# Kernel tuning notes

Measured on AMD Instinct MI355X. Metric: run time of the kernel, lower is better.

Reference implementation:

```python
import jax, jax.numpy as jnp
import numpy as np

B, T, D = 2, 2048, 2048
H, KV, HD = 16, 8, 128
N_REP = H // KV
EPS = 1e-6
ROPE_THETA = 5e6
K_MASK = float(jnp.finfo(jnp.bfloat16).min)


def setup_inputs() -> dict:
    key = jax.random.key(0)
    ks = jax.random.split(key, 8)
    x = jax.random.normal(ks[0], (B, T, D), dtype=jnp.float32)
    wq = jax.random.normal(ks[1], (D, H * HD), dtype=jnp.float32) * 0.02
    wk = jax.random.normal(ks[2], (D, KV * HD), dtype=jnp.float32) * 0.02
    wv = jax.random.normal(ks[3], (D, KV * HD), dtype=jnp.float32) * 0.02
    wo = jax.random.normal(ks[4], (H * HD, D), dtype=jnp.float32) * 0.02
    qn_w = jnp.ones((HD,), dtype=jnp.float32)
    kn_w = jnp.ones((HD,), dtype=jnp.float32)
    # real rotary angles: [T, HD//2] -> broadcast to [B, T, HD//2]
    pos = jnp.arange(T, dtype=jnp.float32)
    inv_freq = 1.0 / (ROPE_THETA ** (jnp.arange(0, HD, 2, dtype=jnp.float32) / HD))
    ang = pos[:, None] * inv_freq[None, :]
    sin = jnp.broadcast_to(jnp.sin(ang)[None], (B, T, HD // 2))
    cos = jnp.broadcast_to(jnp.cos(ang)[None], (B, T, HD // 2))
    # causal mask [B, 1, T, T]
    causal = jnp.tril(jnp.ones((T, T), dtype=jnp.bool_))
    mask = jnp.broadcast_to(causal[None, None], (B, 1, T, T))
    k_cache = jnp.zeros((B, T, KV, HD), dtype=jnp.float32)
    v_cache = jnp.zeros((B, T, KV, HD), dtype=jnp.float32)
    return {"x": x, "wq": wq, "wk": wk, "wv": wv, "wo": wo,
            "qn_w": qn_w, "kn_w": kn_w, "sin": sin, "cos": cos,
            "mask": mask, "k_cache": k_cache, "v_cache": v_cache}


def _rms_norm(h, w):
    h32 = h.astype(jnp.float32)
    rms = jax.lax.rsqrt(jnp.mean(h32 * h32, axis=-1, keepdims=True) + EPS)
    return (h32 * rms * w).astype(h.dtype)


def _apply_rope(x, sin, cos):
    x1, x2 = x[..., : HD // 2], x[..., HD // 2:]
    s, c = sin[:, :, None, :], cos[:, :, None, :]  # [B,T,1,HD/2]
    return jnp.concatenate([x1 * c - x2 * s, x2 * c + x1 * s], axis=-1).astype(x.dtype)


def reference(x, wq, wk, wv, wo, qn_w, kn_w, sin, cos, mask, k_cache, v_cache):
    b, t, _ = x.shape
    q = _rms_norm((x @ wq).reshape(b, t, H, HD), qn_w)
    k = _rms_norm((x @ wk).reshape(b, t, KV, HD), kn_w)
    v = (x @ wv).reshape(b, t, KV, HD)
    q = _apply_rope(q, sin, cos)
    k = _apply_rope(k, sin, cos)
    # KV-cache update at cur_ind = 0 (prefill)
    k_cache = jax.lax.dynamic_update_slice(k_cache, k.astype(k_cache.dtype), (0, 0, 0, 0))
    v_cache = jax.lax.dynamic_update_slice(v_cache, v.astype(v_cache.dtype), (0, 0, 0, 0))
    # GQA repeat_kv: [B,S,KV,HD] -> [B,S,H,HD]
    kf = jnp.repeat(k_cache, N_REP, axis=2)
    vf = jnp.repeat(v_cache, N_REP, axis=2)
    scale = HD ** -0.5
    # [B,H,T,S]
    attn = jnp.einsum('bthd,bshd->bhts', q, kf) * scale
    attn = jnp.where(mask, attn, K_MASK)
    attn = jax.nn.softmax(attn.astype(jnp.float32), axis=-1).astype(q.dtype)
    out = jnp.einsum('bhts,bshd->bthd', attn, vf).reshape(b, t, H * HD)
    return out @ wo
```

## Files before the change

### kernel.cpp

```cpp
#include <hip/hip_runtime.h>
#include <hip/hip_bf16.h>
#include <stdint.h>

#define BB 2
#define TT 2048
#define DD 2048
#define HH 16
#define KVH 8
#define HDIM 128
#define BT (BB*TT)
#define NQKV (HH*HDIM + 2*KVH*HDIM)
#define TQ (TT/128)
#define ATT_SCALE 0.08838834764831845f
#define RMS_EPS 1e-6f

typedef __bf16 bf16;
typedef __bf16 bf16x8 __attribute__((ext_vector_type(8)));
typedef __bf16 bf16x4 __attribute__((ext_vector_type(4)));
typedef __bf16 bf16x2 __attribute__((ext_vector_type(2)));
typedef float  f32x4  __attribute__((ext_vector_type(4)));
typedef float  f32x16 __attribute__((ext_vector_type(16)));
typedef unsigned u32x4 __attribute__((ext_vector_type(4)));

__device__ __forceinline__ void gl_lds16(const void* g, const void* l) {
  __builtin_amdgcn_global_load_lds(
      (const __attribute__((address_space(1))) void*)(uintptr_t)g,
      (__attribute__((address_space(3))) void*)(uint32_t)(uintptr_t)l,
      16, 0, 0);
}

__device__ __forceinline__ unsigned pkbf(float lo, float hi) {
  bf16x2 t = { (bf16)lo, (bf16)hi };
  return __builtin_bit_cast(unsigned, t);
}

__global__ __launch_bounds__(256) void prep_k(const float* __restrict__ x,
                                              const float* __restrict__ wq,
                                              const float* __restrict__ wk,
                                              const float* __restrict__ wv,
                                              const float* __restrict__ wo,
                                              bf16* __restrict__ xb,
                                              bf16* __restrict__ Wt,
                                              bf16* __restrict__ Wot) {
  const int z = blockIdx.z;
  if (z == 0) {
    int id = (blockIdx.y * 32 + blockIdx.x) * 2048 + threadIdx.x;
#pragma unroll
    for (int i = 0; i < 8; ++i) {
      int idx = id + i * 256;
      float4 v = ((const float4*)x)[idx];
      bf16x4 o4 = { (bf16)v.x, (bf16)v.y, (bf16)v.z, (bf16)v.w };
      *(bf16x4*)(xb + (size_t)idx * 4) = o4;
    }
    return;
  }
  const float* in; bf16* out; int C;
  const int R = 2048;
  if (z == 1)      { in = wq; out = Wt;                          C = 2048; }
  else if (z == 2) { in = wk; out = Wt + (size_t)2048 * 2048;    C = 1024; }
  else if (z == 3) { in = wv; out = Wt + (size_t)3072 * 2048;    C = 1024; }
  else             { in = wo; out = Wot;                         C = 2048; }
  int c0 = blockIdx.x * 64, r0 = blockIdx.y * 64;
  if (c0 >= C) return;
  __shared__ float tile[64][65];
  const int lane = threadIdx.x & 63, wid = threadIdx.x >> 6;
#pragma unroll
  for (int i = 0; i < 16; ++i) {
    int rr = wid * 16 + i;
    tile[rr][lane] = in[(size_t)(r0 + rr) * C + c0 + lane];
  }
  __syncthreads();
#pragma unroll
  for (int i = 0; i < 16; ++i) {
    int cc = wid * 16 + i;
    out[(size_t)(c0 + cc) * R + r0 + lane] = (bf16)tile[lane][cc];
  }
}

__global__ __launch_bounds__(256) void transpose_v_k(const bf16* __restrict__ vb,
                                                     bf16* __restrict__ vbt) {
  __shared__ bf16 tile[64][65];
  const int lane = threadIdx.x & 63, wid = threadIdx.x >> 6;
  int t0 = blockIdx.x * 64;
  int d0 = blockIdx.y * 64;
  int bk = blockIdx.z;
  int b = bk >> 3, kv = bk & 7;
#pragma unroll
  for (int i = 0; i < 16; ++i) {
    int rr = wid * 16 + i;
    tile[rr][lane] = vb[(((size_t)(b*TT + t0 + rr)) * KVH + kv) * HDIM + d0 + lane];
  }
  __syncthreads();
#pragma unroll
  for (int i = 0; i < 16; ++i) {
    int cc = wid * 16 + i;
    vbt[(((size_t)bk) * HDIM + d0 + cc) * TT + t0 + lane] = tile[lane][cc];
  }
}

template <int OUT_F32>
__global__ __launch_bounds__(512, 2)
void gemm256_k(const bf16* __restrict__ A, const bf16* __restrict__ Bt,
               void* __restrict__ Cout, int M, int N, int K) {
  __shared__ bf16 S[2 * 2 * 2 * 128 * 64];
  const int tid = threadIdx.x, lane = tid & 63, wid = tid >> 6;
  const int lr = lane & 15, lq = lane >> 4;
  const int wrow = wid >> 1, wcol = wid & 1;

  const int nwg = gridDim.x;
  const int o = blockIdx.x;
  const int ns = (o & 7) * (nwg >> 3) + (o >> 3);
  const int GX = N >> 8;
  const int by = ns / GX, bx = ns % GX;

  const int NT = K >> 6;
  const bf16* Ab = A + (size_t)(by * 256) * K;
  const bf16* Bb = Bt + (size_t)(bx * 256) * K;

  const int srow = tid >> 3;
  const size_t soff = (size_t)srow * K + (((tid & 7) ^ (srow & 7)) * 8);
  const int ldst0 = wid * 512;

  auto STAGE = [&](int op, int h, int t_) {
    int tc = t_ < NT ? t_ : NT - 1;
    const bf16* src = (op ? Bb : Ab) + soff + (size_t)(h * 128) * K + tc * 64;
    bf16* dst = S + ((((((t_ & 1) << 1) | op) << 1) | h) << 13) + ldst0;
#pragma unroll
    for (int i = 0; i < 2; ++i)
      gl_lds16(src + (size_t)(i * 64) * K, dst + i * 4096);
  };

  bf16x8 af[2][2][2];
  bf16x8 bfr[4][2];
  f32x4 acc[4][2][4] = {};

  auto LOAD_A = [&](int buf) {
#pragma unroll
    for (int mh = 0; mh < 2; ++mh) {
      const bf16* base = S + (((buf << 2) | mh) << 13);
#pragma unroll
      for (int m = 0; m < 2; ++m) {
        int ra = wrow * 32 + m * 16 + lr;
#pragma unroll
        for (int ks = 0; ks < 2; ++ks)
          af[mh][m][ks] = *(const bf16x8*)(base + ra * 64 + (((ks * 4 + lq) ^ (ra & 7)) * 8));
      }
    }
  };
  auto LOAD_B = [&](int buf, int nh) {
    const bf16* base = S + (((buf << 2) | 2 | nh) << 13);
#pragma unroll
    for (int n = 0; n < 4; ++n) {
      int rb = wcol * 64 + n * 16 + lr;
#pragma unroll
      for (int ks = 0; ks < 2; ++ks)
        bfr[n][ks] = *(const bf16x8*)(base + rb * 64 + (((ks * 4 + lq) ^ (rb & 7)) * 8));
    }
  };
  auto MFMA_Q = [&](int qd, int mh) {
#pragma unroll
    for (int m = 0; m < 2; ++m)
#pragma unroll
      for (int n = 0; n < 4; ++n)
#pragma unroll
        for (int ks = 0; ks < 2; ++ks)
          acc[qd][m][n] = __builtin_amdgcn_mfma_f32_16x16x32_bf16(
              af[mh][m][ks], bfr[n][ks], acc[qd][m][n], 0, 0, 0);
  };

  STAGE(0, 0, 0); STAGE(0, 1, 0); STAGE(1, 0, 0); STAGE(1, 1, 0);
  STAGE(0, 0, 1); STAGE(0, 1, 1); STAGE(1, 0, 1);
  asm volatile("s_waitcnt vmcnt(6)" ::: "memory");
  __builtin_amdgcn_sched_barrier(0);
  __builtin_amdgcn_s_barrier();

  for (int t = 0; t < NT; ++t) {
    const int buf = t & 1;
    LOAD_A(buf);
    LOAD_B(buf, 0);
    STAGE(1, 1, t + 1);
    __builtin_amdgcn_s_barrier();
    asm volatile("s_waitcnt lgkmcnt(0)" ::: "memory");
    __builtin_amdgcn_sched_barrier(0);
    __builtin_amdgcn_s_setprio(1);
    MFMA_Q(0, 0);
    __builtin_amdgcn_s_setprio(0);
    __builtin_amdgcn_sched_barrier(0);
    __builtin_amdgcn_s_barrier();
    STAGE(0, 0, t + 2);
    __builtin_amdgcn_s_barrier();
    __builtin_amdgcn_s_setprio(1);
    MFMA_Q(1, 1);
    __builtin_amdgcn_s_setprio(0);
    __builtin_amdgcn_sched_barrier(0);
    __builtin_amdgcn_s_barrier();
    LOAD_B(buf, 1);
    STAGE(0, 1, t + 2);
    __builtin_amdgcn_s_barrier();
    asm volatile("s_waitcnt lgkmcnt(0)" ::: "memory");
    __builtin_amdgcn_sched_barrier(0);
    __builtin_amdgcn_s_setprio(1);
    MFMA_Q(2, 1);
    __builtin_amdgcn_s_setprio(0);
    __builtin_amdgcn_sched_barrier(0);
    __builtin_amdgcn_s_barrier();
    STAGE(1, 0, t + 2);
    asm volatile("s_waitcnt vmcnt(6)" ::: "memory");
    __builtin_amdgcn_sched_barrier(0);
    __builtin_amdgcn_s_barrier();
    __builtin_amdgcn_s_setprio(1);
    MFMA_Q(3, 0);
    __builtin_amdgcn_s_setprio(0);
    __builtin_amdgcn_sched_barrier(0);
    __builtin_amdgcn_s_barrier();
  }

#pragma unroll
  for (int qd = 0; qd < 4; ++qd) {
    const int mh = (qd == 1 || qd == 2) ? 1 : 0;
    const int nh = (qd >= 2) ? 1 : 0;
#pragma unroll
    for (int m = 0; m < 2; ++m)
#pragma unroll
      for (int n = 0; n < 4; ++n)
#pragma unroll
        for (int j = 0; j < 4; ++j) {
          int row = by * 256 + mh * 128 + wrow * 32 + m * 16 + lq * 4 + j;
          int col = bx * 256 + nh * 128 + wcol * 64 + n * 16 + lr;
          if (OUT_F32) ((float*)Cout)[(size_t)row * N + col] = acc[qd][m][n][j];
          else         ((bf16*)Cout)[(size_t)row * N + col] = (bf16)acc[qd][m][n][j];
        }
  }
}

template <int OUT_F32>
__global__ __launch_bounds__(512, 1)
void gemm256x128_k(const bf16* __restrict__ A, const bf16* __restrict__ Bt,
                   void* __restrict__ Cout, int M, int N, int K) {
  __shared__ bf16 S[2 * 3 * 128 * 64];
  const int tid = threadIdx.x, lane = tid & 63, wid = tid >> 6;
  const int lr = lane & 15, lq = lane >> 4;
  const int wrow = wid >> 1, wcol = wid & 1;

  const int nwg = gridDim.x;
  const int o = blockIdx.x;
  const int ns = (o & 7) * (nwg >> 3) + (o >> 3);
  const int GX = N >> 7;
  const int by = ns / GX, bx = ns % GX;

  const int NT = K >> 6;
  const bf16* Ab = A + (size_t)(by * 256) * K;
  const bf16* Bb = Bt + (size_t)(bx * 128) * K;

  const int srow = tid >> 3;
  const size_t soff = (size_t)srow * K + (((tid & 7) ^ (srow & 7)) * 8);
  const int ldst0 = wid * 512;

  auto STAGE = [&](int sec, int t_) {
    int tc = t_ < NT ? t_ : NT - 1;
    const bf16* src = (sec == 2 ? Bb : Ab + (size_t)(sec * 128) * K) + soff + tc * 64;
    bf16* dst = S + ((t_ & 1) * 3 + sec) * 8192 + ldst0;
#pragma unroll
    for (int i = 0; i < 2; ++i)
      gl_lds16(src + (size_t)(i * 64) * K, dst + i * 4096);
  };

  bf16x8 af[2][2][2];
  bf16x8 bfr[4][2];
  f32x4 acc[2][2][4] = {};

  auto LOAD_A = [&](int buf) {
#pragma unroll
    for (int mh = 0; mh < 2; ++mh) {
      const bf16* base = S + (buf * 3 + mh) * 8192;
#pragma unroll
      for (int m = 0; m < 2; ++m) {
        int ra = wrow * 32 + m * 16 + lr;
#pragma unroll
        for (int ks = 0; ks < 2; ++ks)
          af[mh][m][ks] = *(const bf16x8*)(base + ra * 64 + (((ks * 4 + lq) ^ (ra & 7)) * 8));
      }
    }
  };
  auto LOAD_B = [&](int buf, int ng) {
    const bf16* base = S + (buf * 3 + 2) * 8192;
#pragma unroll
    for (int n = 2 * ng; n < 2 * ng + 2; ++n) {
      int rb = wcol * 64 + n * 16 + lr;
#pragma unroll
      for (int ks = 0; ks < 2; ++ks)
        bfr[n][ks] = *(const bf16x8*)(base + rb * 64 + (((ks * 4 + lq) ^ (rb & 7)) * 8));
    }
  };
  auto MFMA_Q = [&](int mh, int ng) {
#pragma unroll
    for (int m = 0; m < 2; ++m)
#pragma unroll
      for (int n = 2 * ng; n < 2 * ng + 2; ++n)
#pragma unroll
        for (int ks = 0; ks < 2; ++ks)
          acc[mh][m][n] = __builtin_amdgcn_mfma_f32_16x16x32_bf16(
              af[mh][m][ks], bfr[n][ks], acc[mh][m][n], 0, 0, 0);
  };

  STAGE(0, 0); STAGE(1, 0); STAGE(2, 0);
  STAGE(0, 1); STAGE(1, 1);
  asm volatile("s_waitcnt vmcnt(4)" ::: "memory");
  __builtin_amdgcn_sched_barrier(0);
  __builtin_amdgcn_s_barrier();

  for (int t = 0; t < NT; ++t) {
    const int buf = t & 1;
    LOAD_A(buf);
    LOAD_B(buf, 0);
    STAGE(2, t + 1);
    __builtin_amdgcn_s_barrier();
    asm volatile("s_waitcnt lgkmcnt(0)" ::: "memory");
    __builtin_amdgcn_sched_barrier(0);
    __builtin_amdgcn_s_setprio(1);
    MFMA_Q(0, 0);
    __builtin_amdgcn_s_setprio(0);
    __builtin_amdgcn_sched_barrier(0);
    __builtin_amdgcn_s_barrier();
    STAGE(0, t + 2);
    __builtin_amdgcn_s_barrier();
    __builtin_amdgcn_s_setprio(1);
    MFMA_Q(1, 0);
    __builtin_amdgcn_s_setprio(0);
    __builtin_amdgcn_sched_barrier(0);
    __builtin_amdgcn_s_barrier();
    LOAD_B(buf, 1);
    STAGE(1, t + 2);
    __builtin_amdgcn_s_barrier();
    asm volatile("s_waitcnt lgkmcnt(0)" ::: "memory");
    __builtin_amdgcn_sched_barrier(0);
    __builtin_amdgcn_s_setprio(1);
    MFMA_Q(1, 1);
    __builtin_amdgcn_s_setprio(0);
    __builtin_amdgcn_sched_barrier(0);
    __builtin_amdgcn_s_barrier();
    asm volatile("s_waitcnt vmcnt(4)" ::: "memory");
    __builtin_amdgcn_sched_barrier(0);
    __builtin_amdgcn_s_barrier();
    __builtin_amdgcn_s_setprio(1);
    MFMA_Q(0, 1);
    __builtin_amdgcn_s_setprio(0);
    __builtin_amdgcn_sched_barrier(0);
    __builtin_amdgcn_s_barrier();
  }

#pragma unroll
  for (int mh = 0; mh < 2; ++mh)
#pragma unroll
    for (int m = 0; m < 2; ++m)
#pragma unroll
      for (int n = 0; n < 4; ++n)
#pragma unroll
        for (int j = 0; j < 4; ++j) {
          int row = by * 256 + mh * 128 + wrow * 32 + m * 16 + lq * 4 + j;
          int col = bx * 128 + wcol * 64 + n * 16 + lr;
          if (OUT_F32) ((float*)Cout)[(size_t)row * N + col] = acc[mh][m][n][j];
          else         ((bf16*)Cout)[(size_t)row * N + col] = (bf16)acc[mh][m][n][j];
        }
}

__global__ __launch_bounds__(256) void norm_rope_k(const bf16* __restrict__ qkv,
                                                   const float* __restrict__ qn_w,
                                                   const float* __restrict__ kn_w,
                                                   const float* __restrict__ sinb,
                                                   const float* __restrict__ cosb,
                                                   bf16* __restrict__ qro,
                                                   bf16* __restrict__ kro,
                                                   bf16* __restrict__ vo) {
  const int bt = blockIdx.x;
  const int b = bt >> 11, t = bt & 2047;
  const int tid = threadIdx.x, lane = tid & 63, wid = tid >> 6;
  const bf16* row = qkv + (size_t)bt * NQKV;
  const int fl = (lane & 31) * 2;
  const float2 sv2 = *(const float2*)(sinb + bt * 64 + fl);
  const float2 cv2 = *(const float2*)(cosb + bt * 64 + fl);
  const bool low = lane < 32;
  for (int it = 0; it < 8; ++it) {
    int hv = it * 4 + wid;
    int off = (hv < 16) ? hv * 128 : (hv < 24) ? 2048 + (hv - 16) * 128 : 3072 + (hv - 24) * 128;
    bf16x2 pr = *(const bf16x2*)(row + off + 2 * lane);
    if (hv >= 24) {
      *(bf16x2*)(vo + (size_t)bt * (KVH * HDIM) + (hv - 24) * 128 + 2 * lane) = pr;
    } else {
      float a0 = (float)pr[0], a1 = (float)pr[1];
      float ss = a0 * a0 + a1 * a1;
#pragma unroll
      for (int o = 32; o >= 1; o >>= 1) ss += __shfl_xor(ss, o, 64);
      float rms = rsqrtf(ss * (1.0f / 128.0f) + RMS_EPS);
      const float* wn = (hv < 16) ? qn_w : kn_w;
      float2 w2 = *(const float2*)(wn + 2 * lane);
      float n0 = a0 * rms * w2.x;
      float n1 = a1 * rms * w2.y;
      float p0 = __shfl_xor(n0, 32, 64);
      float p1 = __shfl_xor(n1, 32, 64);
      float o0, o1;
      if (low) { o0 = n0 * cv2.x - p0 * sv2.x; o1 = n1 * cv2.y - p1 * sv2.y; }
      else     { o0 = n0 * cv2.x + p0 * sv2.x; o1 = n1 * cv2.y + p1 * sv2.y; }
      bf16x2 o2 = { (bf16)o0, (bf16)o1 };
      if (hv < 16)
        *(bf16x2*)(qro + (size_t)bt * (HH * HDIM) + hv * 128 + 2 * lane) = o2;
      else
        *(bf16x2*)(kro + (((size_t)b * KVH + (hv - 16)) * TT + t) * HDIM + 2 * lane) = o2;
    }
  }
}

__global__ __launch_bounds__(256, 2)
void attn13_k(const bf16* __restrict__ qr, const bf16* __restrict__ kr2,
              const bf16* __restrict__ vbt, bf16* __restrict__ ao) {
  __shared__ bf16 Ks[2][64 * 128];
  __shared__ bf16 Vs[2][128 * 64];
  const int tid = threadIdx.x, lane = tid & 63, wid = tid >> 6;
  const int l31 = lane & 31, hi = lane >> 5;
  const int h = blockIdx.y, b = blockIdx.z;
  const int qt = (b & 1) ? (TQ - 1 - blockIdx.x) : blockIdx.x;
  const int kvh = h >> 1;
  const int q0w = qt * 128 + wid * 32;
  const int qg = q0w + l31;
  const int nt = 2 * qt + 2;

  const bf16* Kbase = kr2 + ((size_t)(b * KVH + kvh)) * TT * HDIM;
  const bf16* Vbase = vbt + ((size_t)(b * KVH + kvh)) * ((size_t)HDIM * TT);

  auto STAGE = [&](int bufi, int kt) {
#pragma unroll
    for (int i = 0; i < 4; ++i) {
      int u = i * 256 + tid;
      int krow = u >> 4, kcc = u & 15;
      gl_lds16(Kbase + (size_t)(kt * 64 + krow) * HDIM + ((kcc ^ (krow & 15)) * 8),
               &Ks[bufi][(i * 256 + wid * 64) * 8]);
      int vrow = u >> 3, vcc = u & 7;
      gl_lds16(Vbase + (size_t)vrow * TT + kt * 64 + ((vcc ^ (vrow & 7)) * 8),
               &Vs[bufi][(i * 256 + wid * 64) * 8]);
    }
  };

  bf16x8 qf[8];
  const bf16* qrow = &qr[(((size_t)(b * TT + qg)) * HH + h) * HDIM];
#pragma unroll
  for (int ks = 0; ks < 8; ++ks)
    qf[ks] = *(const bf16x8*)(qrow + ks * 16 + hi * 8);

  f32x16 accO[4] = {};
  float m = -INFINITY, lsum = 0.f;
  const float SC2 = ATT_SCALE * 1.4426950408889634f;

  int buf = 0;
  STAGE(0, 0);
  __syncthreads();

  for (int kt = 0; kt < nt; ++kt) {
    if (kt + 1 < nt) STAGE(buf ^ 1, kt + 1);

    if (kt * 64 <= q0w + 31) {
      const char* Kb = (const char*)&Ks[buf][0];
      const char* Vb = (const char*)&Vs[buf][0];
      const bool domask = (kt * 64 + 63) > q0w;

      f32x16 sacc[2];
#pragma unroll
      for (int ct = 0; ct < 2; ++ct) {
#pragma unroll
        for (int j = 0; j < 16; ++j) sacc[ct][j] = 0.f;
        int krow = ct * 32 + l31;
#pragma unroll
        for (int ks = 0; ks < 8; ++ks) {
          bf16x8 kf = *(const bf16x8*)(Kb + krow * 256 + (((2 * ks + hi) ^ (krow & 15)) * 16));
          sacc[ct] = __builtin_amdgcn_mfma_f32_32x32x16_bf16(kf, qf[ks], sacc[ct], 0, 0, 0);
        }
      }

      float p[2][16];
      float pmx = -INFINITY;
      if (domask) {
#pragma unroll
        for (int ct = 0; ct < 2; ++ct) {
          int lim = qg - (kt * 64 + ct * 32 + 4 * hi);
#pragma unroll
          for (int r = 0; r < 16; ++r) {
            const int crow0 = (r & 3) + 8 * (r >> 2);
            float v = sacc[ct][r] * SC2;
            v = (crow0 <= lim) ? v : -INFINITY;
            p[ct][r] = v;
            pmx = fmaxf(pmx, v);
          }
        }
      } else {
#pragma unroll
        for (int ct = 0; ct < 2; ++ct)
#pragma unroll
          for (int r = 0; r < 16; ++r) {
            float v = sacc[ct][r] * SC2;
            p[ct][r] = v;
            pmx = fmaxf(pmx, v);
          }
      }
      pmx = fmaxf(pmx, __shfl_xor(pmx, 32, 64));

      if (__any(pmx > m + 11.54f)) {
        float mnew = fmaxf(m, pmx);
        float alpha = exp2f(m - mnew);
        m = mnew;
        lsum *= alpha;
        int ai = __builtin_bit_cast(int, alpha);
#pragma unroll
        for (int r = 0; r < 16; ++r) {
          const int crow = (r & 3) + 8 * (r >> 2) + 4 * hi;
          float av = __builtin_bit_cast(float, __builtin_amdgcn_ds_bpermute(crow << 2, ai));
#pragma unroll
          for (int n = 0; n < 4; ++n) accO[n][r] *= av;
        }
      }

      float rsum = 0.f;
#pragma unroll
      for (int ct = 0; ct < 2; ++ct)
#pragma unroll
        for (int r = 0; r < 16; ++r) {
          float e = exp2f(p[ct][r] - m);
          p[ct][r] = e;
          rsum += e;
        }
      rsum += __shfl_xor(rsum, 32, 64);
      lsum += rsum;

      bf16x8 pa[4];
#pragma unroll
      for (int ct = 0; ct < 2; ++ct) {
        unsigned W[8];
#pragma unroll
        for (int mi = 0; mi < 8; ++mi)
          W[mi] = pkbf(p[ct][2 * mi], p[ct][2 * mi + 1]);
#pragma unroll
        for (int a = 0; a < 2; ++a) {
          unsigned s0 = __shfl_xor(W[4 * a + 0], 32, 64);
          unsigned s1 = __shfl_xor(W[4 * a + 1], 32, 64);
          unsigned s2 = __shfl_xor(W[4 * a + 2], 32, 64);
          unsigned s3 = __shfl_xor(W[4 * a + 3], 32, 64);
          u32x4 wv;
          wv[0] = hi ? s2 : W[4 * a + 0];
          wv[1] = hi ? s3 : W[4 * a + 1];
          wv[2] = hi ? W[4 * a + 2] : s0;
          wv[3] = hi ? W[4 * a + 3] : s1;
          pa[ct * 2 + a] = __builtin_bit_cast(bf16x8, wv);
        }
      }

#pragma unroll
      for (int n = 0; n < 4; ++n) {
        int vrow = n * 32 + l31;
#pragma unroll
        for (int ks = 0; ks < 4; ++ks) {
          bf16x8 vf = *(const bf16x8*)(Vb + vrow * 128 + (((2 * ks + hi) ^ (vrow & 7)) * 16));
          accO[n] = __builtin_amdgcn_mfma_f32_32x32x16_bf16(pa[ks], vf, accO[n], 0, 0, 0);
        }
      }
    }

    __syncthreads();
    buf ^= 1;
  }

  float inv = 1.0f / lsum;
  int ii = __builtin_bit_cast(int, inv);
#pragma unroll
  for (int n = 0; n < 4; ++n)
#pragma unroll
    for (int r = 0; r < 16; ++r) {
      const int crow = (r & 3) + 8 * (r >> 2) + 4 * hi;
      float av = __builtin_bit_cast(float, __builtin_amdgcn_ds_bpermute(crow << 2, ii));
      size_t idx = (((size_t)(b * TT + q0w + crow)) * HH + h) * HDIM + n * 32 + l31;
      ao[idx] = (bf16)(accO[n][r] * av);
    }
}

extern "C" void kernel_launch(void* const* d_in, const int* in_sizes, int n_in,
                              void* d_out, int out_size, void* d_ws, size_t ws_size,
                              hipStream_t stream) {
  const float* x    = (const float*)d_in[0];
  const float* wq   = (const float*)d_in[1];
  const float* wk   = (const float*)d_in[2];
  const float* wv   = (const float*)d_in[3];
  const float* wo   = (const float*)d_in[4];
  const float* qn_w = (const float*)d_in[5];
  const float* kn_w = (const float*)d_in[6];
  const float* sinb = (const float*)d_in[7];
  const float* cosb = (const float*)d_in[8];
  float* out = (float*)d_out;

  char* ws = (char*)d_ws;
  size_t off = 0;
  auto alloc = [&](size_t bytes) {
    char* p = ws + off;
    off += (bytes + 255) & ~(size_t)255;
    return p;
  };
  bf16* xb  = (bf16*)alloc((size_t)BT * DD * 2);
  bf16* Wt  = (bf16*)alloc((size_t)NQKV * DD * 2);
  bf16* Wot = (bf16*)alloc((size_t)DD * DD * 2);
  bf16* qkv = (bf16*)alloc((size_t)BT * NQKV * 2);
  bf16* kro = (bf16*)alloc((size_t)BT * KVH * HDIM * 2);
  bf16* vb  = (bf16*)alloc((size_t)BT * KVH * HDIM * 2);
  bf16* vbt = (bf16*)alloc((size_t)BT * KVH * HDIM * 2);
  bf16* qro = Wt;
  bf16* aob = xb;
  (void)ws_size; (void)in_sizes; (void)n_in; (void)out_size;

  prep_k<<<dim3(32, 32, 5), 256, 0, stream>>>(x, wq, wk, wv, wo, xb, Wt, Wot);

  gemm256_k<0><<<dim3((BT / 256) * (NQKV / 256)), 512, 0, stream>>>(xb, Wt, qkv, BT, NQKV, DD);

  norm_rope_k<<<BT, 256, 0, stream>>>(qkv, qn_w, kn_w, sinb, cosb, qro, kro, vb);
  transpose_v_k<<<dim3(TT / 64, HDIM / 64, BB * KVH), 256, 0, stream>>>(vb, vbt);

  attn13_k<<<dim3(TQ, HH, BB), 256, 0, stream>>>(qro, kro, vbt, aob);

  gemm256x128_k<1><<<dim3((BT / 256) * (DD / 128)), 512, 0, stream>>>(aob, Wot, out, BT, DD, DD);
}
```

Measured before the change: 210.2 us.

## Fuse RMS norm and RoPE into QKV GEMM epilogue, drop norm_rope kernel

Folds per-head RMS normalization and rotary embedding into the QKV projection GEMM epilogue. Partial sums of squares and partner-half values are exchanged through LDS. V tiles are written directly in a [b,kv,t,d] layout, and the transpose kernel's indexing is updated to match. This removes the intermediate qkv buffer round trip and one kernel launch. In exchange the epilogue gains extra syncs and scattered 2-byte stores.

```diff
diff --git a/kernel.cpp b/kernel.cpp
--- a/kernel.cpp
+++ b/kernel.cpp
@@ -84,11 +84,10 @@
   int t0 = blockIdx.x * 64;
   int d0 = blockIdx.y * 64;
   int bk = blockIdx.z;
-  int b = bk >> 3, kv = bk & 7;
 #pragma unroll
   for (int i = 0; i < 16; ++i) {
     int rr = wid * 16 + i;
-    tile[rr][lane] = vb[(((size_t)(b*TT + t0 + rr)) * KVH + kv) * HDIM + d0 + lane];
+    tile[rr][lane] = vb[((size_t)bk * TT + t0 + rr) * HDIM + d0 + lane];
   }
   __syncthreads();
 #pragma unroll
@@ -98,10 +97,13 @@
   }
 }
 
-template <int OUT_F32>
 __global__ __launch_bounds__(512, 2)
-void gemm256_k(const bf16* __restrict__ A, const bf16* __restrict__ Bt,
-               void* __restrict__ Cout, int M, int N, int K) {
+void gemm256qkv_k(const bf16* __restrict__ A, const bf16* __restrict__ Bt,
+                  bf16* __restrict__ qro, bf16* __restrict__ kro,
+                  bf16* __restrict__ vb,
+                  const float* __restrict__ qn_w, const float* __restrict__ kn_w,
+                  const float* __restrict__ sinb, const float* __restrict__ cosb,
+                  int M, int N, int K) {
   __shared__ bf16 S[2 * 2 * 2 * 128 * 64];
   const int tid = threadIdx.x, lane = tid & 63, wid = tid >> 6;
   const int lr = lane & 15, lq = lane >> 4;
@@ -215,21 +217,94 @@
     __builtin_amdgcn_s_barrier();
   }
 
+  __syncthreads();
+  float* ex  = (float*)S;
+  float* ssb = ex + 16384;
+
+  if (bx >= 12) {
+#pragma unroll
+    for (int qd = 0; qd < 4; ++qd) {
+      const int mh = (qd == 1 || qd == 2) ? 1 : 0;
+      const int nh = (qd >= 2) ? 1 : 0;
+      const int kvh = (bx - 12) * 2 + nh;
+#pragma unroll
+      for (int m = 0; m < 2; ++m)
+#pragma unroll
+        for (int j = 0; j < 4; ++j) {
+          int bt = by * 256 + mh * 128 + wrow * 32 + m * 16 + lq * 4 + j;
+          int bb = bt >> 11, t2 = bt & 2047;
+          bf16* dst = vb + ((size_t)(bb * KVH + kvh) * TT + t2) * HDIM;
+#pragma unroll
+          for (int n = 0; n < 4; ++n)
+            dst[wcol * 64 + n * 16 + lr] = (bf16)acc[qd][m][n][j];
+        }
+    }
+    return;
+  }
+
+  const bool isQ = (bx < 8);
+  const float* wn = isQ ? qn_w : kn_w;
+  float w_own[4], w_par[4];
+#pragma unroll
+  for (int n = 0; n < 4; ++n) {
+    w_own[n] = wn[wcol * 64 + n * 16 + lr];
+    w_par[n] = wn[(wcol ^ 1) * 64 + n * 16 + lr];
+  }
+
 #pragma unroll
   for (int qd = 0; qd < 4; ++qd) {
     const int mh = (qd == 1 || qd == 2) ? 1 : 0;
     const int nh = (qd >= 2) ? 1 : 0;
+    float ssp[2][4];
 #pragma unroll
     for (int m = 0; m < 2; ++m)
 #pragma unroll
+      for (int j = 0; j < 4; ++j) {
+        float s = 0.f;
+#pragma unroll
+        for (int n = 0; n < 4; ++n) { float v = acc[qd][m][n][j]; s += v * v; }
+#pragma unroll
+        for (int off = 1; off < 16; off <<= 1) s += __shfl_xor(s, off, 64);
+        ssp[m][j] = s;
+      }
+    if (lr == 0) {
+#pragma unroll
+      for (int m = 0; m < 2; ++m)
+#pragma unroll
+        for (int j = 0; j < 4; ++j)
+          ssb[wcol * 128 + wrow * 32 + m * 16 + lq * 4 + j] = ssp[m][j];
+    }
+#pragma unroll
+    for (int m = 0; m < 2; ++m)
+#pragma unroll
       for (int n = 0; n < 4; ++n)
 #pragma unroll
-        for (int j = 0; j < 4; ++j) {
-          int row = by * 256 + mh * 128 + wrow * 32 + m * 16 + lq * 4 + j;
-          int col = bx * 256 + nh * 128 + wcol * 64 + n * 16 + lr;
-          if (OUT_F32) ((float*)Cout)[(size_t)row * N + col] = acc[qd][m][n][j];
-          else         ((bf16*)Cout)[(size_t)row * N + col] = (bf16)acc[qd][m][n][j];
-        }
+        for (int j = 0; j < 4; ++j)
+          ex[(m * 16 + n * 4 + j) * 512 + wid * 64 + lane] = acc[qd][m][n][j];
+    __syncthreads();
+
+#pragma unroll
+    for (int m = 0; m < 2; ++m)
+#pragma unroll
+      for (int j = 0; j < 4; ++j) {
+        float tot = ssp[m][j] + ssb[(wcol ^ 1) * 128 + wrow * 32 + m * 16 + lq * 4 + j];
+        float rms = rsqrtf(tot * (1.0f / 128.0f) + RMS_EPS);
+        int bt = by * 256 + mh * 128 + wrow * 32 + m * 16 + lq * 4 + j;
+        int bb = bt >> 11, t2 = bt & 2047;
+        bf16* dst;
+        if (isQ) dst = qro + (size_t)bt * (HH * HDIM) + (bx * 2 + nh) * 128;
+        else     dst = kro + ((size_t)(bb * KVH + (bx - 8) * 2 + nh) * TT + t2) * HDIM;
+#pragma unroll
+        for (int n = 0; n < 4; ++n) {
+          float sv = sinb[bt * 64 + n * 16 + lr];
+          float cv = cosb[bt * 64 + n * 16 + lr];
+          float own = acc[qd][m][n][j] * rms * w_own[n];
+          float par = ex[(m * 16 + n * 4 + j) * 512 + (wid ^ 1) * 64 + lane] * rms * w_par[n];
+          float ov = wcol ? (own * cv + par * sv) : (own * cv - par * sv);
+          dst[wcol * 64 + n * 16 + lr] = (bf16)ov;
+        }
+      }
+    __syncthreads();
   }
 }
 
@@ -364,54 +439,8 @@
         }
 }
 
-__global__ __launch_bounds__(256) void norm_rope_k(const bf16* __restrict__ qkv,
-                                                   const float* __restrict__ qn_w,
-                                                   const float* __restrict__ kn_w,
-                                                   const float* __restrict__ sinb,
-                                                   const float* __restrict__ cosb,
-                                                   bf16* __restrict__ qro,
-                                                   bf16* __restrict__ kro,
-                                                   bf16* __restrict__ vo) {
-  const int bt = blockIdx.x;
-  const int b = bt >> 11, t = bt & 2047;
-  const int tid = threadIdx.x, lane = tid & 63, wid = tid >> 6;
-  const bf16* row = qkv + (size_t)bt * NQKV;
-  const int fl = (lane & 31) * 2;
-  const float2 sv2 = *(const float2*)(sinb + bt * 64 + fl);
-  const float2 cv2 = *(const float2*)(cosb + bt * 64 + fl);
-  const bool low = lane < 32;
-  for (int it = 0; it < 8; ++it) {
-    int hv = it * 4 + wid;
-    int off = (hv < 16) ? hv * 128 : (hv < 24) ? 2048 + (hv - 16) * 128 : 3072 + (hv - 24) * 128;
-    bf16x2 pr = *(const bf16x2*)(row + off + 2 * lane);
-    if (hv >= 24) {
-      *(bf16x2*)(vo + (size_t)bt * (KVH * HDIM) + (hv - 24) * 128 + 2 * lane) = pr;
-    } else {
-      float a0 = (float)pr[0], a1 = (float)pr[1];
-      float ss = a0 * a0 + a1 * a1;
-#pragma unroll
-      for (int o = 32; o >= 1; o >>= 1) ss += __shfl_xor(ss, o, 64);
-      float rms = rsqrtf(ss * (1.0f / 128.0f) + RMS_EPS);
-      const float* wn = (hv < 16) ? qn_w : kn_w;
-      float2 w2 = *(const float2*)(wn + 2 * lane);
-      float n0 = a0 * rms * w2.x;
-      float n1 = a1 * rms * w2.y;
-      float p0 = __shfl_xor(n0, 32, 64);
-      float p1 = __shfl_xor(n1, 32, 64);
-      float o0, o1;
-      if (low) { o0 = n0 * cv2.x - p0 * sv2.x; o1 = n1 * cv2.y - p1 * sv2.y; }
-      else     { o0 = n0 * cv2.x + p0 * sv2.x; o1 = n1 * cv2.y + p1 * sv2.y; }
-      bf16x2 o2 = { (bf16)o0, (bf16)o1 };
-      if (hv < 16)
-        *(bf16x2*)(qro + (size_t)bt * (HH * HDIM) + hv * 128 + 2 * lane) = o2;
-      else
-        *(bf16x2*)(kro + (((size_t)b * KVH + (hv - 16)) * TT + t) * HDIM + 2 * lane) = o2;
-    }
-  }
-}
-
 __global__ __launch_bounds__(256, 2)
-void attn13_k(const bf16* __restrict__ qr, const bf16* __restrict__ kr2,
+void attn14_k(const bf16* __restrict__ qr, const bf16* __restrict__ kr2,
               const bf16* __restrict__ vbt, bf16* __restrict__ ao) {
   __shared__ bf16 Ks[2][64 * 128];
   __shared__ bf16 Vs[2][128 * 64];
@@ -603,22 +632,21 @@
   bf16* xb  = (bf16*)alloc((size_t)BT * DD * 2);
   bf16* Wt  = (bf16*)alloc((size_t)NQKV * DD * 2);
   bf16* Wot = (bf16*)alloc((size_t)DD * DD * 2);
-  bf16* qkv = (bf16*)alloc((size_t)BT * NQKV * 2);
+  bf16* qro = (bf16*)alloc((size_t)BT * HH * HDIM * 2);
   bf16* kro = (bf16*)alloc((size_t)BT * KVH * HDIM * 2);
   bf16* vb  = (bf16*)alloc((size_t)BT * KVH * HDIM * 2);
   bf16* vbt = (bf16*)alloc((size_t)BT * KVH * HDIM * 2);
-  bf16* qro = Wt;
   bf16* aob = xb;
   (void)ws_size; (void)in_sizes; (void)n_in; (void)out_size;
 
   prep_k<<<dim3(32, 32, 5), 256, 0, stream>>>(x, wq, wk, wv, wo, xb, Wt, Wot);
 
-  gemm256_k<0><<<dim3((BT / 256) * (NQKV / 256)), 512, 0, stream>>>(xb, Wt, qkv, BT, NQKV, DD);
-
-  norm_rope_k<<<BT, 256, 0, stream>>>(qkv, qn_w, kn_w, sinb, cosb, qro, kro, vb);
+  gemm256qkv_k<<<dim3((BT / 256) * (NQKV / 256)), 512, 0, stream>>>(
+      xb, Wt, qro, kro, vb, qn_w, kn_w, sinb, cosb, BT, NQKV, DD);
+
   transpose_v_k<<<dim3(TT / 64, HDIM / 64, BB * KVH), 256, 0, stream>>>(vb, vbt);
 
-  attn13_k<<<dim3(TQ, HH, BB), 256, 0, stream>>>(qro, kro, vbt, aob);
+  attn14_k<<<dim3(TQ, HH, BB), 256, 0, stream>>>(qro, kro, vbt, aob);
 
   gemm256x128_k<1><<<dim3((BT / 256) * (DD / 128)), 512, 0, stream>>>(aob, Wot, out, BT, DD, DD);
 }
```

Result: faster. 205.0 us (-2.5%).
